# Kernel optimization log

Measured on AMD Instinct MI355X. Metric: run time of the kernel, lower is better.

Reference implementation:

```python
import jax, jax.numpy as jnp
import numpy as np

B, S = 32, 256          # sequences, tokens per sequence (prefill)
DIM, NH, NKV, HD = 2048, 16, 16, 128
CLS, GRID, BASE = 1, 16, 10000


def precompute_freqs_cis_2d(grid_size, n_elem, base, cls_token_num):
    half = n_elem // 2
    freqs = 1.0 / (base ** (np.arange(0, half, 2)[: half // 2].astype(np.float32) / half))
    t = np.arange(grid_size, dtype=np.float32)
    fr = np.outer(t, freqs)                      # [grid, half//2]
    fg = np.concatenate([
        np.broadcast_to(fr[:, None, :], (grid_size, grid_size, fr.shape[1])),
        np.broadcast_to(fr[None, :, :], (grid_size, grid_size, fr.shape[1])),
    ], axis=-1)                                  # [grid, grid, half]
    cache = np.stack([np.cos(fg), np.sin(fg)], axis=-1).reshape(grid_size * grid_size, half, 2)
    cond = np.concatenate([np.zeros((cls_token_num, half, 2), np.float32), cache.astype(np.float32)], axis=0)
    return jnp.asarray(cond)                     # [cls+grid^2, half, 2]

FREQS = precompute_freqs_cis_2d(GRID, HD, BASE, CLS)


def _apply_rope(x, fc):
    # x: [T, H, HD], fc: [T, HD//2, 2]
    xr = x.reshape(x.shape[0], x.shape[1], HD // 2, 2)
    c = fc[:, None, :, 0]
    s = fc[:, None, :, 1]
    out = jnp.stack([xr[..., 0] * c - xr[..., 1] * s,
                     xr[..., 1] * c + xr[..., 0] * s], axis=-1)
    return out.reshape(x.shape)


def setup_inputs() -> dict:
    key = jax.random.key(0)
    k1, k2, k3 = jax.random.split(key, 3)
    x = jax.random.normal(k1, (B * S, DIM), dtype=jnp.float32)
    positions = jnp.tile(jnp.arange(S, dtype=jnp.int32), B)  # per-seq positions 0..S-1
    total_kv = (NH + 2 * NKV) * HD
    wqkv = jax.random.normal(k2, (total_kv, DIM), dtype=jnp.float32) * 0.02
    wo = jax.random.normal(k3, (DIM, DIM), dtype=jnp.float32) * 0.02
    return {"x": x, "positions": positions, "wqkv": wqkv, "wo": wo}


def reference(x, positions, wqkv, wo):
    T = x.shape[0]
    kv_size = NKV * HD
    qkv = x @ wqkv.T                               # [T, dim + 2*kv_size]
    xq, xk, xv = jnp.split(qkv, [DIM, DIM + kv_size], axis=-1)
    q = xq.reshape(T, NH, HD)
    k = xk.reshape(T, NKV, HD)
    v = xv.reshape(T, NKV, HD)

    fc = FREQS[positions]                          # [T, HD//2, 2]
    q = _apply_rope(q, fc)
    k = _apply_rope(k, fc)

    # paged attention (prefill): causal attention within each sequence
    qb = q.reshape(B, S, NH, HD)
    kb = k.reshape(B, S, NKV, HD)
    vb = v.reshape(B, S, NKV, HD)
    scale = HD ** -0.5
    scores = jnp.einsum("bqhd,bkhd->bhqk", qb, kb) * scale   # [B,H,S,S]
    causal = jnp.tril(jnp.ones((S, S), dtype=bool))
    scores = jnp.where(causal[None, None], scores, jnp.finfo(scores.dtype).min)
    attn = jax.nn.softmax(scores, axis=-1)
    out = jnp.einsum("bhqk,bkhd->bqhd", attn, vb).reshape(T, DIM)
    return out @ wo.T
```

## Files before the change

kernel.cpp:

```cpp
#include <hip/hip_runtime.h>
#include <cstddef>


typedef float    f32x4 __attribute__((ext_vector_type(4)));
typedef _Float16 f16x8 __attribute__((ext_vector_type(8)));
typedef _Float16 f16x4 __attribute__((ext_vector_type(4)));

#define LOG2E 1.4426950408889634f
#define NLOG2B_32 (-0.41524101186192697f)

__device__ static inline f32x4 mfma16x32(f16x8 a, f16x8 b, f32x4 c) {
  return __builtin_amdgcn_mfma_f32_16x16x32_f16(a, b, c, 0, 0, 0);
}

__device__ static inline void gload16(const void* g, void* lds) {
  __builtin_amdgcn_global_load_lds(
      (const __attribute__((address_space(1))) unsigned int*)g,
      (__attribute__((address_space(3))) unsigned int*)lds, 16, 0, 0);
}

#define BAR()    asm volatile("s_barrier" ::: "memory")
#define VMCNT6() asm volatile("s_waitcnt vmcnt(6)" ::: "memory")

__global__ void cvt3_f32_f16(const float* __restrict__ s0, _Float16* __restrict__ d0,
                             const float* __restrict__ s1, _Float16* __restrict__ d1,
                             const float* __restrict__ s2, _Float16* __restrict__ d2) {
  int i = blockIdx.x * blockDim.x + threadIdx.x;
  const float* src; _Float16* dst;
  if (i < 4194304)      { src = s0; dst = d0; }
  else if (i < 7340032) { src = s1; dst = d1; i -= 4194304; }
  else                  { src = s2; dst = d2; i -= 7340032; }
  f32x4 v = *(const f32x4*)(src + (size_t)i * 4);
  f16x4 o;
  o[0] = (_Float16)v[0]; o[1] = (_Float16)v[1];
  o[2] = (_Float16)v[2]; o[3] = (_Float16)v[3];
  *(f16x4*)(dst + (size_t)i * 4) = o;
}

template <typename OutT>
__global__ void __launch_bounds__(512, 2)
gemm_bt5(const _Float16* __restrict__ A, const _Float16* __restrict__ Bt,
         OutT* __restrict__ C, int M, int N, int K) {
  __shared__ __attribute__((aligned(16))) _Float16 Ab[2][256 * 64];
  __shared__ __attribute__((aligned(16))) _Float16 Bb[2][256 * 64];

  const int tid  = threadIdx.x;
  const int lane = tid & 63;
  const int w    = tid >> 6;
  const int wm   = w >> 2, wn = w & 3;
  const int g    = lane >> 4, li = lane & 15;

  const int nwg = (int)gridDim.x;
  const int cpx = nwg >> 3;
  const int bid = (int)blockIdx.x;
  const int swz = (bid & 7) * cpx + (bid >> 3);
  const int nbn = N >> 8;
  const int bm  = (swz / nbn) << 8;
  const int bn  = (swz % nbn) << 8;
  const int NT  = K >> 6;

  const int srow = tid >> 3;
  const int scol = ((tid & 7) ^ (srow & 7)) * 8;
  const _Float16* gA = A  + (size_t)(bm + srow) * K + scol;
  const _Float16* gB = Bt + (size_t)(bn + srow) * K + scol;
  const int sdst = w * 1024;

  auto stage = [&](const _Float16* gbase, _Float16* lbase, int h, int kt) {
    const _Float16* gp = gbase + (size_t)h * 128 * K + kt;
    char* lp = (char*)lbase + h * 16384;
#pragma unroll
    for (int j = 0; j < 2; ++j)
      gload16(gp + (size_t)j * 64 * K, lp + j * 8192 + sdst);
  };

  auto rdfrag = [&](const _Float16* buf, int row, int k2) -> f16x8 {
    const int pc = ((k2 << 2) + g) ^ (li & 7);
    return *(const f16x8*)((const char*)buf + row * 128 + pc * 16);
  };

  f32x4 acc[8][4] = {};

  stage(gA, Ab[0], 0, 0);
  stage(gB, Bb[0], 0, 0);
  stage(gB, Bb[0], 1, 0);
  stage(gA, Ab[0], 1, 0);
  stage(gA, Ab[1], 0, (NT > 1) ? 64 : 0);
  VMCNT6();
  BAR();

  for (int T = 0; T < NT; ++T) {
    const int cb = T & 1, nb = cb ^ 1;
    const _Float16* Ac = Ab[cb];
    const _Float16* Bc = Bb[cb];
    const int ktN  = (T + 1 < NT) ? (T + 1) << 6 : 0;
    const int ktN2 = (T + 2 < NT) ? (T + 2) << 6 : 0;

    f16x8 af0[4][2], af1[4][2], bf0[2][2], bf1[2][2];

#pragma unroll
    for (int m = 0; m < 4; ++m)
#pragma unroll
      for (int k2 = 0; k2 < 2; ++k2)
        af0[m][k2] = rdfrag(Ac, wm * 128 + m * 16 + li, k2);
#pragma unroll
    for (int n = 0; n < 2; ++n)
#pragma unroll
      for (int k2 = 0; k2 < 2; ++k2)
        bf0[n][k2] = rdfrag(Bc, wn * 64 + n * 16 + li, k2);
    stage(gB, Bb[nb], 0, ktN);
    __builtin_amdgcn_s_setprio(1);
#pragma unroll
    for (int m = 0; m < 4; ++m)
#pragma unroll
      for (int n = 0; n < 2; ++n)
#pragma unroll
        for (int k2 = 0; k2 < 2; ++k2)
          acc[m][n] = mfma16x32(af0[m][k2], bf0[n][k2], acc[m][n]);
    __builtin_amdgcn_s_setprio(0);
    VMCNT6();
    BAR();

#pragma unroll
    for (int n = 0; n < 2; ++n)
#pragma unroll
      for (int k2 = 0; k2 < 2; ++k2)
        bf1[n][k2] = rdfrag(Bc, wn * 64 + (n + 2) * 16 + li, k2);
    stage(gB, Bb[nb], 1, ktN);
    __builtin_amdgcn_s_setprio(1);
#pragma unroll
    for (int m = 0; m < 4; ++m)
#pragma unroll
      for (int n = 0; n < 2; ++n)
#pragma unroll
        for (int k2 = 0; k2 < 2; ++k2)
          acc[m][n + 2] = mfma16x32(af0[m][k2], bf1[n][k2], acc[m][n + 2]);
    __builtin_amdgcn_s_setprio(0);
    VMCNT6();
    BAR();

#pragma unroll
    for (int m = 0; m < 4; ++m)
#pragma unroll
      for (int k2 = 0; k2 < 2; ++k2)
        af1[m][k2] = rdfrag(Ac, wm * 128 + (m + 4) * 16 + li, k2);
    stage(gA, Ab[nb], 1, ktN);
    __builtin_amdgcn_s_setprio(1);
#pragma unroll
    for (int m = 0; m < 4; ++m)
#pragma unroll
      for (int n = 0; n < 2; ++n)
#pragma unroll
        for (int k2 = 0; k2 < 2; ++k2)
          acc[m + 4][n] = mfma16x32(af1[m][k2], bf0[n][k2], acc[m + 4][n]);
    __builtin_amdgcn_s_setprio(0);
    VMCNT6();
    BAR();

    stage(gA, Ab[cb], 0, ktN2);
    __builtin_amdgcn_s_setprio(1);
#pragma unroll
    for (int m = 0; m < 4; ++m)
#pragma unroll
      for (int n = 0; n < 2; ++n)
#pragma unroll
        for (int k2 = 0; k2 < 2; ++k2)
          acc[m + 4][n + 2] = mfma16x32(af1[m][k2], bf1[n][k2], acc[m + 4][n + 2]);
    __builtin_amdgcn_s_setprio(0);
    VMCNT6();
    BAR();
  }

  asm volatile("s_waitcnt vmcnt(0)" ::: "memory");

#pragma unroll
  for (int m = 0; m < 8; ++m)
#pragma unroll
    for (int n = 0; n < 4; ++n)
#pragma unroll
      for (int r = 0; r < 4; ++r) {
        const int row = bm + wm * 128 + m * 16 + g * 4 + r;
        const int col = bn + wn * 64 + n * 16 + li;
        C[(size_t)row * N + col] = (OutT)acc[m][n][r];
      }
}

__global__ void __launch_bounds__(512)
attn_kernel(const _Float16* __restrict__ qkv, _Float16* __restrict__ O,
            const int* __restrict__ positions) {
  const int b  = blockIdx.x >> 4;
  const int h  = blockIdx.x & 15;
  const int tb = b << 8;
  const int tid = threadIdx.x;
  const int lane = tid & 63;
  const int w = tid >> 6;
  const int g = lane >> 4, li = lane & 15;

  __shared__ __attribute__((aligned(16))) _Float16 Ks[64 * 128];
  __shared__ __attribute__((aligned(16))) _Float16 Vt[128 * 64];
  __shared__ __attribute__((aligned(16))) _Float16 Ps[8][32 * 40];
  __shared__ float2 tab[512];
  __shared__ int    ptab[256];

  {
    const float ang = (float)(tid >> 5) * exp2f((float)(tid & 31) * NLOG2B_32);
    float s, c;
    sincosf(ang, &s, &c);
    tab[tid] = make_float2(c, s);
    if (tid < 256) ptab[tid] = positions[tb + tid];
  }
  __syncthreads();

  const int qb[2]   = {w, 15 - w};
  const int qrow[2] = {qb[0] * 16, qb[1] * 16};
  const int kmax[2] = {qb[0] >> 2, qb[1] >> 2};

  f16x8 qf[2][4];
#pragma unroll
  for (int rb = 0; rb < 2; ++rb) {
    const int pos = ptab[qrow[rb] + li];
    const int iv = (pos - 1) >> 4, jv = (pos - 1) & 15;
#pragma unroll
    for (int ks = 0; ks < 4; ++ks) {
      f16x8 v = *(const f16x8*)(qkv + (size_t)(tb + qrow[rb] + li) * 6144
                                + h * 128 + ks * 32 + g * 8);
      f16x8 o;
      if (pos == 0) {
#pragma unroll
        for (int u = 0; u < 8; ++u) o[u] = (_Float16)0.f;
      } else {
        const int tv = (ks < 2) ? iv : jv;
#pragma unroll
        for (int u = 0; u < 4; ++u) {
          const float2 cs = tab[tv * 32 + ((ks * 16 + g * 4 + u) & 31)];
          const float x0 = (float)v[2 * u], x1 = (float)v[2 * u + 1];
          o[2 * u]     = (_Float16)(x0 * cs.x - x1 * cs.y);
          o[2 * u + 1] = (_Float16)(x1 * cs.x + x0 * cs.y);
        }
      }
      qf[rb][ks] = o;
    }
  }

  f32x4 oacc[2][8] = {};
  float m_r[2][4], l_r[2][4];
#pragma unroll
  for (int rb = 0; rb < 2; ++rb)
#pragma unroll
    for (int r = 0; r < 4; ++r) { m_r[rb][r] = -1e30f; l_r[rb][r] = 0.f; }

  const float scale = 0.08838834764831845f;

  for (int kt = 0; kt < 4; ++kt) {
#pragma unroll
    for (int i = 0; i < 2; ++i) {
      const int s = i * 512 + tid;
      const int key = s >> 4;
      const int c   = s & 15;
      f16x8 v = *(const f16x8*)(qkv + (size_t)(tb + kt * 64 + key) * 6144
                                + 2048 + h * 128 + c * 8);
      const int pos = ptab[kt * 64 + key];
      f16x8 o;
      if (pos == 0) {
#pragma unroll
        for (int u = 0; u < 8; ++u) o[u] = (_Float16)0.f;
      } else {
        const int iv = (pos - 1) >> 4, jv = (pos - 1) & 15;
        const int tv = (c < 8) ? iv : jv;
#pragma unroll
        for (int u = 0; u < 4; ++u) {
          const float2 cs = tab[tv * 32 + ((c * 4 + u) & 31)];
          const float x0 = (float)v[2 * u], x1 = (float)v[2 * u + 1];
          o[2 * u]     = (_Float16)(x0 * cs.x - x1 * cs.y);
          o[2 * u + 1] = (_Float16)(x1 * cs.x + x0 * cs.y);
        }
      }
      *(f16x8*)((char*)Ks + key * 256 + (c ^ (key & 7)) * 16) = o;
    }
#pragma unroll
    for (int i = 0; i < 2; ++i) {
      const int s = i * 512 + tid;
      const int key = s >> 4;
      const int chv = s & 15;
      f16x8 v = *(const f16x8*)(qkv + (size_t)(tb + kt * 64 + key) * 6144
                                + 4096 + h * 128 + chv * 8);
#pragma unroll
      for (int e = 0; e < 8; ++e) {
        const int d = chv * 8 + e;
        const int blk = ((key >> 3) ^ (d & 7) ^ ((d >> 3) & 7)) & 7;
        Vt[d * 64 + blk * 8 + (key & 7)] = v[e];
      }
    }
    __syncthreads();

    const bool act[2] = {kt <= kmax[0], kt <= kmax[1]};
    if (act[0] || act[1]) {
      f32x4 sacc[2][4] = {};
#pragma unroll
      for (int ks = 0; ks < 4; ++ks) {
        f16x8 kf[4];
#pragma unroll
        for (int cb = 0; cb < 4; ++cb) {
          const int key = cb * 16 + li;
          const int chunk = (ks * 4 + g) ^ (key & 7);
          kf[cb] = *(const f16x8*)((const char*)Ks + key * 256 + chunk * 16);
        }
#pragma unroll
        for (int rb = 0; rb < 2; ++rb)
          if (act[rb])
#pragma unroll
            for (int cb = 0; cb < 4; ++cb)
              sacc[rb][cb] = mfma16x32(qf[rb][ks], kf[cb], sacc[rb][cb]);
      }
#pragma unroll
      for (int rb = 0; rb < 2; ++rb) {
        if (!act[rb]) continue;
#pragma unroll
        for (int r = 0; r < 4; ++r) {
          const int q = qrow[rb] + g * 4 + r;
          float mx = -1e30f;
#pragma unroll
          for (int cb = 0; cb < 4; ++cb) {
            float sv = sacc[rb][cb][r] * scale;
            const int key = kt * 64 + cb * 16 + li;
            sv = (key <= q) ? sv : -1e30f;
            sacc[rb][cb][r] = sv;
            mx = fmaxf(mx, sv);
          }
#pragma unroll
          for (int off = 1; off < 16; off <<= 1)
            mx = fmaxf(mx, __shfl_xor(mx, off));
          const float mold = m_r[rb][r];
          const float mnew = fmaxf(mold, mx);
          const float alpha = exp2f((mold - mnew) * LOG2E);
          float rsum = 0.f;
#pragma unroll
          for (int cb = 0; cb < 4; ++cb) {
            const float pv = exp2f((sacc[rb][cb][r] - mnew) * LOG2E);
            sacc[rb][cb][r] = pv;
            rsum += pv;
          }
#pragma unroll
          for (int off = 1; off < 16; off <<= 1)
            rsum += __shfl_xor(rsum, off);
          m_r[rb][r] = mnew;
          l_r[rb][r] = l_r[rb][r] * alpha + rsum;
#pragma unroll
          for (int db = 0; db < 8; ++db)
            oacc[rb][db][r] *= alpha;
        }
      }
#pragma unroll
      for (int ks2 = 0; ks2 < 2; ++ks2) {
#pragma unroll
        for (int rb = 0; rb < 2; ++rb) {
          if (!act[rb]) continue;
#pragma unroll
          for (int cbh = 0; cbh < 2; ++cbh) {
            const int cb = ks2 * 2 + cbh;
#pragma unroll
            for (int r = 0; r < 4; ++r)
              Ps[w][(rb * 16 + g * 4 + r) * 40 + cbh * 16 + li] =
                  (_Float16)sacc[rb][cb][r];
          }
        }
        asm volatile("s_waitcnt lgkmcnt(0)" ::: "memory");
        f16x8 pa[2];
#pragma unroll
        for (int rb = 0; rb < 2; ++rb)
          if (act[rb])
            pa[rb] = *(const f16x8*)(&Ps[w][(rb * 16 + li) * 40 + g * 8]);
#pragma unroll
        for (int db = 0; db < 8; ++db) {
          const int d = db * 16 + li;
          const int keych = ks2 * 4 + g;
          const int blk = (keych ^ (d & 7) ^ ((d >> 3) & 7)) & 7;
          const f16x8 vf = *(const f16x8*)(&Vt[d * 64 + blk * 8]);
#pragma unroll
          for (int rb = 0; rb < 2; ++rb)
            if (act[rb])
              oacc[rb][db] = mfma16x32(pa[rb], vf, oacc[rb][db]);
        }
      }
    }
    __syncthreads();
  }
#pragma unroll
  for (int rb = 0; rb < 2; ++rb)
#pragma unroll
    for (int db = 0; db < 8; ++db)
#pragma unroll
      for (int r = 0; r < 4; ++r) {
        const int row = tb + qrow[rb] + g * 4 + r;
        const int col = h * 128 + db * 16 + li;
        O[(size_t)row * 2048 + col] = (_Float16)(oacc[rb][db][r] / l_r[rb][r]);
      }
}

extern "C" void kernel_launch(void* const* d_in, const int* in_sizes, int n_in,
                              void* d_out, int out_size, void* d_ws, size_t ws_size,
                              hipStream_t stream) {
  const float* x         = (const float*)d_in[0];
  const int*   positions = (const int*)d_in[1];
  const float* wqkv      = (const float*)d_in[2];
  const float* wo        = (const float*)d_in[3];
  float* out = (float*)d_out;

  char* ws = (char*)d_ws;
  _Float16* qkv    = (_Float16*)(ws);
  _Float16* xf     = (_Float16*)(ws + 100663296);
  _Float16* wqkvf  = (_Float16*)(ws + 134217728);
  _Float16* wof    = (_Float16*)(ws + 159383552);
  _Float16* of     = xf;

  cvt3_f32_f16<<<32768, 256, 0, stream>>>(x, xf, wqkv, wqkvf, wo, wof);

  gemm_bt5<_Float16><<<768, 512, 0, stream>>>(xf, wqkvf, qkv, 8192, 6144, 2048);

  attn_kernel<<<512, 512, 0, stream>>>(qkv, of, positions);

  gemm_bt5<float><<<256, 512, 0, stream>>>(of, wof, out, 8192, 2048, 2048);
}
```

Baseline: 346.2 us.

## Load V directly to LDS and read transposed via ds_read_b64_tr_b16

Replaces the register-staged scalar transpose of V into LDS with direct global-to-LDS loads (global_load_lds) into a row-major swizzled layout. The B operand for the PV MFMA is now read with the transposing LDS read instruction ds_read_b64_tr_b16, so the eight scattered 2-byte LDS stores per element are gone. All V reads are issued first, then one explicit wait, then the MFMAs. This relies on the swizzle and lane mapping matching the MFMA operand layout, and on the barrier ordering the async LDS loads.

Result: no change. 346.0 us (-0.1%).

```diff
diff --git a/kernel.cpp b/kernel.cpp
--- a/kernel.cpp
+++ b/kernel.cpp
@@ -196,7 +196,7 @@
   const int g = lane >> 4, li = lane & 15;
 
   __shared__ __attribute__((aligned(16))) _Float16 Ks[64 * 128];
-  __shared__ __attribute__((aligned(16))) _Float16 Vt[128 * 64];
+  __shared__ __attribute__((aligned(16))) _Float16 Vt[64 * 128];
   __shared__ __attribute__((aligned(16))) _Float16 Ps[8][32 * 40];
   __shared__ float2 tab[512];
   __shared__ int    ptab[256];
@@ -214,6 +214,11 @@
   const int qrow[2] = {qb[0] * 16, qb[1] * 16};
   const int kmax[2] = {qb[0] >> 2, qb[1] >> 2};
 
+  const int jj = li >> 2;
+  const int cc = li & 3;
+  const unsigned vbase =
+      (unsigned)(unsigned long long)(__attribute__((address_space(3))) _Float16*)Vt;
+
   f16x8 qf[2][4];
 #pragma unroll
   for (int rb = 0; rb < 2; ++rb) {
@@ -251,6 +256,15 @@
   const float scale = 0.08838834764831845f;
 
   for (int kt = 0; kt < 4; ++kt) {
+#pragma unroll
+    for (int i = 0; i < 2; ++i) {
+      const int s = i * 512 + tid;
+      const int key = s >> 4;
+      const int sch = (s & 15) ^ (key & 7);
+      const _Float16* gv = qkv + (size_t)(tb + kt * 64 + key) * 6144
+                           + 4096 + h * 128 + sch * 8;
+      gload16(gv, (char*)Vt + (i * 512 + (tid & ~63)) * 16);
+    }
 #pragma unroll
     for (int i = 0; i < 2; ++i) {
       const int s = i * 512 + tid;
@@ -276,20 +290,6 @@
       }
       *(f16x8*)((char*)Ks + key * 256 + (c ^ (key & 7)) * 16) = o;
     }
-#pragma unroll
-    for (int i = 0; i < 2; ++i) {
-      const int s = i * 512 + tid;
-      const int key = s >> 4;
-      const int chv = s & 15;
-      f16x8 v = *(const f16x8*)(qkv + (size_t)(tb + kt * 64 + key) * 6144
-                                + 4096 + h * 128 + chv * 8);
-#pragma unroll
-      for (int e = 0; e < 8; ++e) {
-        const int d = chv * 8 + e;
-        const int blk = ((key >> 3) ^ (d & 7) ^ ((d >> 3) & 7)) & 7;
-        Vt[d * 64 + blk * 8 + (key & 7)] = v[e];
-      }
-    }
     __syncthreads();
 
     const bool act[2] = {kt <= kmax[0], kt <= kmax[1]};
@@ -369,12 +369,25 @@
         for (int rb = 0; rb < 2; ++rb)
           if (act[rb])
             pa[rb] = *(const f16x8*)(&Ps[w][(rb * 16 + li) * 40 + g * 8]);
+
+        f16x4 vlo[8], vhi[8];
+        const int rowA = ks2 * 32 + g * 8 + jj;
+        const unsigned base1 = vbase + (unsigned)(rowA * 256 + (cc & 1) * 8);
+        const unsigned base2 = base1 + 4 * 256;
 #pragma unroll
         for (int db = 0; db < 8; ++db) {
-          const int d = db * 16 + li;
-          const int keych = ks2 * 4 + g;
-          const int blk = (keych ^ (d & 7) ^ ((d >> 3) & 7)) & 7;
-          const f16x8 vf = *(const f16x8*)(&Vt[d * 64 + blk * 8]);
+          const int ch = db * 2 + (cc >> 1);
+          const unsigned a1 = base1 + (unsigned)((ch ^ jj) << 4);
+          const unsigned a2 = base2 + (unsigned)((ch ^ jj ^ 4) << 4);
+          asm volatile("ds_read_b64_tr_b16 %0, %1" : "=v"(vlo[db]) : "v"(a1));
+          asm volatile("ds_read_b64_tr_b16 %0, %1" : "=v"(vhi[db]) : "v"(a2));
+        }
+        asm volatile("s_waitcnt lgkmcnt(0)" ::: "memory");
+        __builtin_amdgcn_sched_barrier(0);
+#pragma unroll
+        for (int db = 0; db < 8; ++db) {
+          const f16x8 vf = __builtin_shufflevector(vlo[db], vhi[db],
+                                                   0, 1, 2, 3, 4, 5, 6, 7);
 #pragma unroll
           for (int rb = 0; rb < 2; ++rb)
             if (act[rb])
```
